# Kernel tuning notes

Hardware: AMD Instinct MI355X
Metric: run time of the kernel (lower is better)

## Reference

```python
import jax, jax.numpy as jnp
import numpy as np

N = 50000          # nodes
DEG = 8            # per-node in/out degree
E = N * DEG        # fwd edges (rev = reversed fwd)
H = 128            # hidden_dim
T = 4              # towers
F = H // T         # per-tower F_in (divide_input=True)
FO = H // T        # per-tower F_out
L = 2              # num_layers
IN_DIM = 128
OUT_DIM = 32
AVG_LOG = float(np.log(DEG + 1.0))  # avg of log(deg+1) from deg histogram (all deg==8)
BN_EPS = 1e-5
STD_EPS = 1e-5


def setup_inputs() -> dict:
    key = jax.random.key(0)
    ks = jax.random.split(key, 10)
    x = jax.random.normal(ks[0], (N, IN_DIM), jnp.float32)
    # every node appears exactly DEG times as dst and as src -> deg histogram delta at 8
    dst = jnp.repeat(jnp.arange(N, dtype=jnp.int32), DEG)
    src = jax.random.permutation(ks[1], dst)
    edge_fwd = jnp.stack([src, dst])  # [2, E]

    def rn(k, shape):
        return jax.random.normal(k, shape, jnp.float32) * 0.05

    return dict(
        x=x,
        W_in=rn(ks[2], (IN_DIM, H)), b_in=jnp.zeros((H,), jnp.float32),
        # [layer, relation(fwd/rev), tower, ...]
        pre_W=rn(ks[3], (L, 2, T, 2 * F, F)), pre_b=jnp.zeros((L, 2, T, F), jnp.float32),
        post_W=rn(ks[4], (L, 2, T, 13 * F, FO)), post_b=jnp.zeros((L, 2, T, FO), jnp.float32),
        lin_W=rn(ks[5], (L, 2, H, H)), lin_b=jnp.zeros((L, 2, H), jnp.float32),
        bn_gamma=jnp.ones((L, H), jnp.float32), bn_beta=jnp.zeros((L, H), jnp.float32),
        mlp_W1=rn(ks[6], (H, H)), mlp_b1=jnp.zeros((H,), jnp.float32),
        mlp_W2=rn(ks[7], (H, OUT_DIM)), mlp_b2=jnp.zeros((OUT_DIM,), jnp.float32),
        edge_fwd=edge_fwd,
    )


def _pna(x, src, dst, pre_W, pre_b, post_W, post_b, lin_W, lin_b):
    """One PNAConv (divide_input=True, pre/post_layers=1, no edge attr)."""
    xt = x.reshape(N, T, F)                                   # [N,T,F]
    # message: cat([x_i (dst), x_j (src)]) -> per-tower pre-MLP
    h = jnp.concatenate([xt[dst], xt[src]], axis=-1)          # [E,T,2F]
    m = jnp.einsum('etf,tfg->etg', h, pre_W) + pre_b          # [E,T,F]
    # multi-aggregator scatter reduce over destination nodes
    deg = jax.ops.segment_sum(jnp.ones((m.shape[0],), x.dtype), dst, N)
    degc = jnp.maximum(deg, 1.0)
    inv = (1.0 / degc)[:, None, None]
    mean = jax.ops.segment_sum(m, dst, N) * inv
    mean2 = jax.ops.segment_sum(m * m, dst, N) * inv
    std = jnp.sqrt(jax.nn.relu(mean2 - mean * mean) + STD_EPS)
    mn = jax.ops.segment_min(m, dst, N)
    mx = jax.ops.segment_max(m, dst, N)
    agg = jnp.concatenate([mean, mn, mx, std], axis=-1)       # [N,T,4F]
    # degree scalers: amplification, attenuation, identity
    ld = jnp.log(degc + 1.0)[:, None, None]
    agg = jnp.concatenate([agg * (ld / AVG_LOG), agg * (AVG_LOG / ld), agg], axis=-1)  # [N,T,12F]
    out = jnp.concatenate([xt, agg], axis=-1)                 # [N,T,13F]
    out = jnp.einsum('ntf,tfg->ntg', out, post_W) + post_b    # [N,T,FO]
    out = out.reshape(N, T * FO)
    return out @ lin_W + lin_b                                # [N,H]


def _bn(x, g, b):
    mu = x.mean(0)
    var = x.var(0)  # biased, as torch BatchNorm normalization
    return g * (x - mu) * jax.lax.rsqrt(var + BN_EPS) + b


def reference(x, W_in, b_in, pre_W, pre_b, post_W, post_b, lin_W, lin_b,
              bn_gamma, bn_beta, mlp_W1, mlp_b1, mlp_W2, mlp_b2, edge_fwd):
    src, dst = edge_fwd[0], edge_fwd[1]
    h = jax.nn.relu(x @ W_in + b_in)
    for l in range(L):
        # HeteroConv sum of fwd relation and rev relation (reversed edges)
        y = (_pna(h, src, dst, pre_W[l, 0], pre_b[l, 0], post_W[l, 0], post_b[l, 0], lin_W[l, 0], lin_b[l, 0])
             + _pna(h, dst, src, pre_W[l, 1], pre_b[l, 1], post_W[l, 1], post_b[l, 1], lin_W[l, 1], lin_b[l, 1]))
        h = jax.nn.relu(_bn(y, bn_gamma[l], bn_beta[l]))
        # dropout omitted (deterministic reference / eval mode)
    return jax.nn.relu(h @ mlp_W1 + mlp_b1) @ mlp_W2 + mlp_b2
```

## Files before the change

### kernel.cpp

```cpp
#include <hip/hip_runtime.h>
#include <hip/hip_fp16.h>
#include <cstddef>
#include <cstdint>

#define NN 50000
#define DEG 8
#define EE (NN*DEG)
#define RT_CNT 3125
#define KSTEPS 36
#define W8L 18432
#define MPAD 132

typedef __attribute__((ext_vector_type(8))) short short8;
typedef __attribute__((ext_vector_type(4))) float f32x4;

union Pack8 { __half h[8]; __half2 h2[4]; uint4 u; short8 s8; };

__global__ void k_build_nbr(const int* __restrict__ ef, int* __restrict__ cnt,
                            int* __restrict__ fwd_nbr, int* __restrict__ rev_nbr) {
    int e = blockIdx.x * blockDim.x + threadIdx.x;
    if (e >= EE) return;
    int s = ef[e], d = ef[EE + e];
    int p = atomicAdd(&cnt[d], 1);
    fwd_nbr[d * DEG + p] = s;
    int q = atomicAdd(&cnt[NN + s], 1);
    rev_nbr[s * DEG + q] = d;
}

__global__ __launch_bounds__(256) void k_wprep(
    const float* __restrict__ post_W, const float* __restrict__ pre_W,
    const float* __restrict__ pre_b, const float* __restrict__ post_b,
    const float* __restrict__ lin_W, const float* __restrict__ lin_b,
    __half* __restrict__ Wcp, float* __restrict__ Qw, float* __restrict__ bc) {
    __shared__ float Pf[160 * 33];
    __shared__ float Wl[32 * 128];
    __shared__ float Wt[32 * 32];
    __shared__ float Ps[32 * 32];
    __shared__ float Q[32 * 32];
    __shared__ float T3s[32];
    int tid = threadIdx.x;
    int m4 = blockIdx.x;
    int l = m4 >> 3, r = (m4 >> 2) & 1, tw = m4 & 3;
    const float* PW = post_W + (size_t)m4 * 416 * 32;
    for (int i = tid; i < 160 * 32; i += 256) {
        int row = i >> 5, g = i & 31;
        float v;
        if (row < 32) v = PW[row * 32 + g];
        else {
            int rr = row - 32;
            v = PW[(32 + rr) * 32 + g] + PW[(160 + rr) * 32 + g] + PW[(288 + rr) * 32 + g];
        }
        Pf[row * 33 + g] = v;
    }
    for (int i = tid; i < 1024; i += 256) Wt[i] = pre_W[(size_t)m4 * 2048 + i];
    for (int i = tid; i < 4096; i += 256)
        Wl[i] = lin_W[(size_t)(l * 2 + r) * 16384 + tw * 32 * 128 + i];
    __syncthreads();
    for (int i = tid; i < 1024; i += 256) {
        int g = i >> 5, j = i & 31;
        Ps[i] = Pf[(32 + g) * 33 + j] + Pf[(64 + g) * 33 + j] + Pf[(96 + g) * 33 + j];
    }
    __syncthreads();
    for (int i = tid; i < 1024; i += 256) {
        int f = i >> 5, j = i & 31;
        float acc = Pf[f * 33 + j];
#pragma unroll
        for (int g = 0; g < 32; g++) acc += Wt[f * 32 + g] * Ps[g * 32 + j];
        Q[i] = acc;
    }
    if (tid < 32) {
        int j = tid;
        float v = post_b[m4 * 32 + j];
#pragma unroll
        for (int g = 0; g < 32; g++) v += pre_b[m4 * 32 + g] * Ps[g * 32 + j];
        T3s[j] = v;
    }
    __syncthreads();
    for (int u = tid; u < 2048; u += 256) {
        int lane = u & 63, t = (u >> 6) & 7, s = u >> 9;
        int quad = lane >> 4, nl = lane & 15;
        int n = t * 16 + nl;
        Pack8 pk;
#pragma unroll
        for (int e = 0; e < 8; e++) {
            int f = quad * 8 + e;
            const float* Pr = &Pf[((s + 1) * 32 + f) * 33];
            float acc = 0.f;
#pragma unroll
            for (int j = 0; j < 32; j++) acc += Pr[j] * Wl[j * 128 + n];
            pk.h[e] = __float2half(acc);
        }
        int ks = 4 + r * 16 + tw * 4 + s;
        *(uint4*)&Wcp[((size_t)l * W8L + (t * KSTEPS + ks) * 64 + lane) * 8] = pk.u;
    }
    for (int i = tid; i < 4096; i += 256) {
        int f = i >> 7, n = i & 127;
        float acc = 0.f;
#pragma unroll
        for (int j = 0; j < 32; j++) acc += Q[f * 32 + j] * Wl[j * 128 + n];
        atomicAdd(&Qw[(size_t)l * 16384 + (tw * 32 + f) * 128 + n], acc);
    }
    if (tid < 128) {
        float v = 0.f;
#pragma unroll
        for (int j = 0; j < 32; j++) v += T3s[j] * Wl[j * 128 + tid];
        atomicAdd(&bc[l * 128 + tid], v);
        if ((m4 & 7) == 0)
            atomicAdd(&bc[l * 128 + tid],
                      lin_b[(2 * l) * 128 + tid] + lin_b[(2 * l + 1) * 128 + tid]);
    }
}

__global__ void k_pack_xt(const float* __restrict__ Qw, __half* __restrict__ Wcp) {
    int gid = blockIdx.x * blockDim.x + threadIdx.x;
    if (gid >= 2 * 4 * 8 * 64) return;
    int lane = gid & 63, t = (gid >> 6) & 7, ks = (gid >> 9) & 3, l = gid >> 11;
    int quad = lane >> 4;
    int n = t * 16 + (lane & 15);
    Pack8 pk;
#pragma unroll
    for (int e = 0; e < 8; e++)
        pk.h[e] = __float2half(Qw[(size_t)l * 16384 + (ks * 32 + quad * 8 + e) * 128 + n]);
    *(uint4*)&Wcp[((size_t)l * W8L + (t * KSTEPS + ks) * 64 + lane) * 8] = pk.u;
}

__global__ void k_pack_b(const float* __restrict__ W, int K, int N,
                         __half* __restrict__ dst) {
    int gid = blockIdx.x * blockDim.x + threadIdx.x;
    int total = (K >> 5) * (N >> 4) * 64;
    if (gid >= total) return;
    int lane = gid & 63;
    int ks = (gid >> 6) % (K >> 5);
    int t = (gid >> 6) / (K >> 5);
    int quad = lane >> 4, nl = lane & 15;
    int n = t * 16 + nl;
    Pack8 pk;
#pragma unroll
    for (int e = 0; e < 8; e++)
        pk.h[e] = __float2half(W[(size_t)(ks * 32 + quad * 8 + e) * N + n]);
    *(uint4*)&dst[(size_t)gid * 8] = pk.u;
}

__global__ void k_pack_wbd(const float* __restrict__ pre_W, __half* __restrict__ dst) {
    int gid = blockIdx.x * blockDim.x + threadIdx.x;
    if (gid >= 2 * 2 * 8 * 4 * 64) return;
    int lane = gid & 63, ks = (gid >> 6) & 3, t8 = (gid >> 8) & 7;
    int rel = (gid >> 11) & 1, l = gid >> 12;
    int quad = lane >> 4, nl = lane & 15;
    int n = t8 * 16 + nl;
    int tn = n >> 5;
    Pack8 pk;
#pragma unroll
    for (int e = 0; e < 8; e++) {
        int k = ks * 32 + quad * 8 + e;
        float v = 0.f;
        if ((k >> 5) == tn)
            v = pre_W[(size_t)((((l * 2 + rel) * 4 + tn) * 64) + 32 + (k & 31)) * 32 + (n & 31)];
        pk.h[e] = __float2half(v);
    }
    *(uint4*)&dst[((size_t)(l * 2 + rel) * 2048 + (t8 * 4 + ks) * 64 + lane) * 8] = pk.u;
}

__global__ __launch_bounds__(256) void k_in_mfma(
    const float* __restrict__ X, const __half* __restrict__ Wp,
    const float* __restrict__ b, __half* __restrict__ H) {
    __shared__ __half Sh[4][16 * MPAD];
    int tid = threadIdx.x, wv = tid >> 6, lane = tid & 63;
    int rt = blockIdx.x * 4 + wv;
    if (rt >= RT_CNT) rt = RT_CNT - 1;
    int mm = lane & 15, quad = lane >> 4;
    short8 a[4];
#pragma unroll
    for (int ks = 0; ks < 4; ks++) {
        const float4* p = (const float4*)&X[(size_t)(rt * 16 + mm) * 128 + ks * 32 + quad * 8];
        float4 v0 = p[0], v1 = p[1];
        Pack8 pk;
        pk.h[0] = __float2half(v0.x); pk.h[1] = __float2half(v0.y);
        pk.h[2] = __float2half(v0.z); pk.h[3] = __float2half(v0.w);
        pk.h[4] = __float2half(v1.x); pk.h[5] = __float2half(v1.y);
        pk.h[6] = __float2half(v1.z); pk.h[7] = __float2half(v1.w);
        a[ks] = pk.s8;
    }
    const short8* Bb = (const short8*)Wp + lane;
    f32x4 acc[8];
#pragma unroll
    for (int t = 0; t < 8; t++) acc[t] = (f32x4){0.f, 0.f, 0.f, 0.f};
#pragma unroll
    for (int ks = 0; ks < 4; ks++)
#pragma unroll
        for (int t = 0; t < 8; t++)
            acc[t] = __builtin_amdgcn_mfma_f32_16x16x32_f16(
                a[ks], Bb[(t * 4 + ks) * 64], acc[t], 0, 0, 0);
    __half* T = Sh[wv];
#pragma unroll
    for (int t = 0; t < 8; t++) {
        int n = t * 16 + mm;
        float bias = b[n];
#pragma unroll
        for (int r = 0; r < 4; r++)
            T[(quad * 4 + r) * MPAD + n] = __float2half(fmaxf(acc[t][r] + bias, 0.f));
    }
#pragma unroll
    for (int it = 0; it < 4; it++) {
        int idx = it * 64 + lane;
        int row = idx >> 4, col = (idx & 15) * 8;
        *(uint4*)&H[(size_t)(rt * 16 + row) * 128 + col] = *(uint4*)&T[row * MPAD + col];
    }
}

template<int V>
__global__ __launch_bounds__(256) void k_preB_mfma(
    const __half* __restrict__ Hin, const float* __restrict__ Yf,
    const float* __restrict__ bns, const float* __restrict__ bns2,
    const float* __restrict__ gamma, const float* __restrict__ beta,
    __half* __restrict__ Hout, const __half* __restrict__ WbBDp,
    __half* __restrict__ Bplanes) {
    __shared__ __half Sh[4][16 * MPAD];
    __shared__ float sc[128], sh[128];
    int tid = threadIdx.x, wv = tid >> 6, lane = tid & 63;
    int rt = blockIdx.x * 4 + wv;
    if (rt >= RT_CNT) rt = RT_CNT - 1;
    if (V == 2) {
        if (tid < 128) {
            float mu = bns[tid] * (1.f / NN);
            float var = bns2[tid] * (1.f / NN) - mu * mu;
            float s = gamma[tid] * rsqrtf(var + 1e-5f);
            sc[tid] = s;
            sh[tid] = beta[tid] - mu * s;
        }
        __syncthreads();
    }
    int mm = lane & 15, quad = lane >> 4;
    short8 a[4];
#pragma unroll
    for (int ks = 0; ks < 4; ks++) {
        int c0 = ks * 32 + quad * 8;
        size_t base = (size_t)(rt * 16 + mm) * 128 + c0;
        if (V == 1) {
            Pack8 pk; pk.u = *(const uint4*)&Hin[base];
            a[ks] = pk.s8;
        } else {
            const float4* p = (const float4*)&Yf[base];
            float4 v0 = p[0], v1 = p[1];
            float4 s0 = *(const float4*)&sc[c0], s1 = *(const float4*)&sc[c0 + 4];
            float4 f0 = *(const float4*)&sh[c0], f1 = *(const float4*)&sh[c0 + 4];
            Pack8 pk;
            pk.h[0] = __float2half(fmaxf(s0.x * v0.x + f0.x, 0.f));
            pk.h[1] = __float2half(fmaxf(s0.y * v0.y + f0.y, 0.f));
            pk.h[2] = __float2half(fmaxf(s0.z * v0.z + f0.z, 0.f));
            pk.h[3] = __float2half(fmaxf(s0.w * v0.w + f0.w, 0.f));
            pk.h[4] = __float2half(fmaxf(s1.x * v1.x + f1.x, 0.f));
            pk.h[5] = __float2half(fmaxf(s1.y * v1.y + f1.y, 0.f));
            pk.h[6] = __float2half(fmaxf(s1.z * v1.z + f1.z, 0.f));
            pk.h[7] = __float2half(fmaxf(s1.w * v1.w + f1.w, 0.f));
            *(uint4*)&Hout[base] = pk.u;
            a[ks] = pk.s8;
        }
    }
    __half* T = Sh[wv];
#pragma unroll
    for (int rel = 0; rel < 2; rel++) {
        const short8* Bb = (const short8*)WbBDp + (size_t)rel * 2048 + lane;
        f32x4 acc[8];
#pragma unroll
        for (int t = 0; t < 8; t++) acc[t] = (f32x4){0.f, 0.f, 0.f, 0.f};
#pragma unroll
        for (int ks = 0; ks < 4; ks++)
#pragma unroll
            for (int t = 0; t < 8; t++)
                acc[t] = __builtin_amdgcn_mfma_f32_16x16x32_f16(
                    a[ks], Bb[(t * 4 + ks) * 64], acc[t], 0, 0, 0);
#pragma unroll
        for (int t = 0; t < 8; t++) {
            int n = t * 16 + mm;
#pragma unroll
            for (int r = 0; r < 4; r++)
                T[(quad * 4 + r) * MPAD + n] = __float2half(acc[t][r]);
        }
        __half* Bp = Bplanes + (size_t)rel * NN * 128;
#pragma unroll
        for (int it = 0; it < 4; it++) {
            int idx = it * 64 + lane;
            int row = idx >> 4, col = (idx & 15) * 8;
            *(uint4*)&Bp[(size_t)(rt * 16 + row) * 128 + col] = *(uint4*)&T[row * MPAD + col];
        }
    }
}

__global__ __launch_bounds__(256, 4) void k_agg_gemm(
    const __half* __restrict__ hbuf, const __half* __restrict__ Bplanes,
    const int* __restrict__ fwd_nbr, const int* __restrict__ rev_nbr,
    const __half* __restrict__ Wcp, const float* __restrict__ bc,
    float* __restrict__ Y, float* __restrict__ bnsum, float* __restrict__ bnsum2) {
    __shared__ __half Spack[KSTEPS * 64 * 8];
    __shared__ float bnred[256];
    int tid = threadIdx.x;
    int blk = blockIdx.x;
    bnred[tid] = 0.f;
    int lane = tid & 63, wv = tid >> 6;
    int s = lane >> 4, f16 = lane & 15;
    int tw = f16 >> 2, quad = f16 & 3;
    int m = wv * 4 + s;
    int d = blk * 16 + m;
    {
        const int4* nf = (const int4*)&fwd_nbr[d * 8];
        const int4* nr = (const int4*)&rev_nbr[d * 8];
        int4 a0 = nf[0], a1 = nf[1], b0v = nr[0], b1v = nr[1];
        int idx0[8] = {a0.x, a0.y, a0.z, a0.w, a1.x, a1.y, a1.z, a1.w};
        int idx1[8] = {b0v.x, b0v.y, b0v.z, b0v.w, b1v.x, b1v.y, b1v.z, b1v.w};
        int fo = f16 * 8;
        Pack8 r0[8], r1[8];
        const __half* Bp1 = Bplanes + (size_t)NN * 128;
#pragma unroll
        for (int k = 0; k < 8; k++)
            r0[k].u = *(const uint4*)&Bplanes[(size_t)idx0[k] * 128 + fo];
#pragma unroll
        for (int k = 0; k < 8; k++)
            r1[k].u = *(const uint4*)&Bp1[(size_t)idx1[k] * 128 + fo];
        Pack8 xr;
        xr.u = *(const uint4*)&hbuf[(size_t)(blk * 16 + f16) * 128 + wv * 32 + s * 8];
        int pos = 16 * quad + (m ^ quad ^ ((tw & 1) << 2));
#pragma unroll
        for (int rel = 0; rel < 2; rel++) {
            Pack8* rr = rel ? r1 : r0;
            float sS[8], qS[8], mnS[8], mxS[8];
#pragma unroll
            for (int j = 0; j < 8; j++) {
                sS[j] = 0.f; qS[j] = 0.f; mnS[j] = 1e30f; mxS[j] = -1e30f;
            }
#pragma unroll
            for (int k = 0; k < 8; k++) {
#pragma unroll
                for (int j2 = 0; j2 < 4; j2++) {
                    __half2 h = rr[k].h2[j2];
                    float a = __half2float(__low2half(h));
                    float b = __half2float(__high2half(h));
                    int j0 = 2 * j2, j1 = j0 + 1;
                    sS[j0] += a; qS[j0] += a * a;
                    mnS[j0] = fminf(mnS[j0], a); mxS[j0] = fmaxf(mxS[j0], a);
                    sS[j1] += b; qS[j1] += b * b;
                    mnS[j1] = fminf(mnS[j1], b); mxS[j1] = fmaxf(mxS[j1], b);
                }
            }
            Pack8 mean, stdv, mnp, mxp;
#pragma unroll
            for (int j = 0; j < 8; j++) {
                float Bm = sS[j] * 0.125f;
                mean.h[j] = __float2half(Bm);
                stdv.h[j] = __float2half(
                    sqrtf(fmaxf(qS[j] * 0.125f - Bm * Bm, 0.f) + 1e-5f));
                mnp.h[j] = __float2half(mnS[j]);
                mxp.h[j] = __float2half(mxS[j]);
            }
            int ksb = 4 + rel * 16 + tw * 4;
            *(uint4*)&Spack[((size_t)(ksb + 0) * 64 + pos) * 8] = mean.u;
            *(uint4*)&Spack[((size_t)(ksb + 1) * 64 + pos) * 8] = mnp.u;
            *(uint4*)&Spack[((size_t)(ksb + 2) * 64 + pos) * 8] = mxp.u;
            *(uint4*)&Spack[((size_t)(ksb + 3) * 64 + pos) * 8] = stdv.u;
        }
        int posx = 16 * s + (f16 ^ s ^ ((wv & 1) << 2));
        *(uint4*)&Spack[((size_t)wv * 64 + posx) * 8] = xr.u;
    }
    __syncthreads();
    int mB = lane & 15, qB = lane >> 4;
    int t0 = wv * 2;
    const short8* Bb = (const short8*)Wcp + lane;
    f32x4 acc0 = (f32x4){0.f, 0.f, 0.f, 0.f};
    f32x4 acc1 = (f32x4){0.f, 0.f, 0.f, 0.f};
    short8 p0[6], p1[6];
#pragma unroll
    for (int dd = 0; dd < 6; dd++) {
        p0[dd] = Bb[((size_t)t0 * KSTEPS + dd) * 64];
        p1[dd] = Bb[((size_t)(t0 + 1) * KSTEPS + dd) * 64];
    }
#pragma unroll
    for (int ks = 0; ks < KSTEPS; ks++) {
        int twk = (ks < 4) ? ks : (((ks - 4) >> 2) & 3);
        int posr = 16 * qB + (mB ^ qB ^ ((twk & 1) << 2));
        short8 a = *(const short8*)&Spack[((size_t)ks * 64 + posr) * 8];
        acc0 = __builtin_amdgcn_mfma_f32_16x16x32_f16(a, p0[ks % 6], acc0, 0, 0, 0);
        acc1 = __builtin_amdgcn_mfma_f32_16x16x32_f16(a, p1[ks % 6], acc1, 0, 0, 0);
        if (ks + 6 < KSTEPS) {
            p0[ks % 6] = Bb[((size_t)t0 * KSTEPS + ks + 6) * 64];
            p1[ks % 6] = Bb[((size_t)(t0 + 1) * KSTEPS + ks + 6) * 64];
        }
    }
#pragma unroll
    for (int tt = 0; tt < 2; tt++) {
        f32x4 acc = tt ? acc1 : acc0;
        int n = (t0 + tt) * 16 + mB;
        float bias = bc[n];
        float ls = 0.f, ls2 = 0.f;
#pragma unroll
        for (int r = 0; r < 4; r++) {
            float v = acc[r] + bias;
            int node = blk * 16 + qB * 4 + r;
            Y[(size_t)node * 128 + n] = v;
            ls += v; ls2 += v * v;
        }
        ls += __shfl_xor(ls, 16); ls += __shfl_xor(ls, 32);
        ls2 += __shfl_xor(ls2, 16); ls2 += __shfl_xor(ls2, 32);
        if (qB == 0) { bnred[n] += ls; bnred[128 + n] += ls2; }
    }
    __syncthreads();
    if (tid < 128) {
        atomicAdd(&bnsum[tid], bnred[tid]);
        atomicAdd(&bnsum2[tid], bnred[128 + tid]);
    }
}

__global__ __launch_bounds__(256) void k_mlp_mfma(
    const float* __restrict__ Yb, const float* __restrict__ bns,
    const float* __restrict__ bns2, const float* __restrict__ gamma,
    const float* __restrict__ beta, const __half* __restrict__ W1p,
    const float* __restrict__ b1, const __half* __restrict__ W2p,
    const float* __restrict__ b2, float* __restrict__ out) {
    __shared__ __half Sh[4][16 * MPAD];
    __shared__ float sc[128], sh[128];
    int tid = threadIdx.x, wv = tid >> 6, lane = tid & 63;
    int rt = blockIdx.x * 4 + wv;
    if (rt >= RT_CNT) rt = RT_CNT - 1;
    if (tid < 128) {
        float mu = bns[tid] * (1.f / NN);
        float var = bns2[tid] * (1.f / NN) - mu * mu;
        float s = gamma[tid] * rsqrtf(var + 1e-5f);
        sc[tid] = s;
        sh[tid] = beta[tid] - mu * s;
    }
    __syncthreads();
    int mm = lane & 15, quad = lane >> 4;
    short8 a[4];
#pragma unroll
    for (int ks = 0; ks < 4; ks++) {
        int c0 = ks * 32 + quad * 8;
        const float4* p = (const float4*)&Yb[(size_t)(rt * 16 + mm) * 128 + c0];
        float4 v0 = p[0], v1 = p[1];
        float4 s0 = *(const float4*)&sc[c0], s1 = *(const float4*)&sc[c0 + 4];
        float4 f0 = *(const float4*)&sh[c0], f1 = *(const float4*)&sh[c0 + 4];
        Pack8 pk;
        pk.h[0] = __float2half(fmaxf(s0.x * v0.x + f0.x, 0.f));
        pk.h[1] = __float2half(fmaxf(s0.y * v0.y + f0.y, 0.f));
        pk.h[2] = __float2half(fmaxf(s0.z * v0.z + f0.z, 0.f));
        pk.h[3] = __float2half(fmaxf(s0.w * v0.w + f0.w, 0.f));
        pk.h[4] = __float2half(fmaxf(s1.x * v1.x + f1.x, 0.f));
        pk.h[5] = __float2half(fmaxf(s1.y * v1.y + f1.y, 0.f));
        pk.h[6] = __float2half(fmaxf(s1.z * v1.z + f1.z, 0.f));
        pk.h[7] = __float2half(fmaxf(s1.w * v1.w + f1.w, 0.f));
        a[ks] = pk.s8;
    }
    const short8* B1 = (const short8*)W1p + lane;
    f32x4 acc[8];
#pragma unroll
    for (int t = 0; t < 8; t++) acc[t] = (f32x4){0.f, 0.f, 0.f, 0.f};
#pragma unroll
    for (int ks = 0; ks < 4; ks++)
#pragma unroll
        for (int t = 0; t < 8; t++)
            acc[t] = __builtin_amdgcn_mfma_f32_16x16x32_f16(
                a[ks], B1[(t * 4 + ks) * 64], acc[t], 0, 0, 0);
    __half* T = Sh[wv];
#pragma unroll
    for (int t = 0; t < 8; t++) {
        int n = t * 16 + mm;
        float bias = b1[n];
#pragma unroll
        for (int r = 0; r < 4; r++)
            T[(quad * 4 + r) * MPAD + n] = __float2half(fmaxf(acc[t][r] + bias, 0.f));
    }
    short8 a2[4];
#pragma unroll
    for (int ks = 0; ks < 4; ks++)
        a2[ks] = *(const short8*)&T[mm * MPAD + ks * 32 + quad * 8];
    const short8* B2 = (const short8*)W2p + lane;
    f32x4 acc2[2];
#pragma unroll
    for (int t = 0; t < 2; t++) acc2[t] = (f32x4){0.f, 0.f, 0.f, 0.f};
#pragma unroll
    for (int ks = 0; ks < 4; ks++)
#pragma unroll
        for (int t = 0; t < 2; t++)
            acc2[t] = __builtin_amdgcn_mfma_f32_16x16x32_f16(
                a2[ks], B2[(t * 4 + ks) * 64], acc2[t], 0, 0, 0);
#pragma unroll
    for (int t = 0; t < 2; t++) {
        int n = t * 16 + mm;
        float bias = b2[n];
#pragma unroll
        for (int r = 0; r < 4; r++)
            out[(size_t)(rt * 16 + quad * 4 + r) * 32 + n] = acc2[t][r] + bias;
    }
}

extern "C" void kernel_launch(void* const* d_in, const int* in_sizes, int n_in,
                              void* d_out, int out_size, void* d_ws, size_t ws_size,
                              hipStream_t stream) {
    const float* x      = (const float*)d_in[0];
    const float* W_in   = (const float*)d_in[1];
    const float* b_in   = (const float*)d_in[2];
    const float* pre_W  = (const float*)d_in[3];
    const float* pre_b  = (const float*)d_in[4];
    const float* post_W = (const float*)d_in[5];
    const float* post_b = (const float*)d_in[6];
    const float* lin_W  = (const float*)d_in[7];
    const float* lin_b  = (const float*)d_in[8];
    const float* bn_g   = (const float*)d_in[9];
    const float* bn_b   = (const float*)d_in[10];
    const float* mlp_W1 = (const float*)d_in[11];
    const float* mlp_b1 = (const float*)d_in[12];
    const float* mlp_W2 = (const float*)d_in[13];
    const float* mlp_b2 = (const float*)d_in[14];
    const int*   edge   = (const int*)d_in[15];
    float* out = (float*)d_out;

    char* w = (char*)d_ws;
    const size_t plane = (size_t)NN * 128 * sizeof(float);
    __half* hbuf = (__half*)w; w += plane / 2;
    float* ybuf = (float*)w; w += plane;
    __half* Bpl = (__half*)w; w += plane;
    int* fwd_nbr = (int*)w; w += (size_t)NN * DEG * sizeof(int);
    int* rev_nbr = (int*)w; w += (size_t)NN * DEG * sizeof(int);
    int* cnt     = (int*)w; w += (size_t)2 * NN * sizeof(int);
    float* Qw    = (float*)w; w += (size_t)2 * 128 * 128 * sizeof(float);
    float* bc    = (float*)w; w += 2 * 128 * sizeof(float);
    __half* Wcp  = (__half*)w; w += (size_t)2 * KSTEPS * 32 * 128 * sizeof(__half);
    __half* Winp = (__half*)w; w += (size_t)128 * 128 * sizeof(__half);
    __half* W1p  = (__half*)w; w += (size_t)128 * 128 * sizeof(__half);
    __half* W2p  = (__half*)w; w += (size_t)128 * 32 * sizeof(__half);
    __half* WbBD = (__half*)w; w += (size_t)4 * 128 * 128 * sizeof(__half);
    float* bns   = (float*)w; w += 4 * 128 * sizeof(float);

    const int gWave = (RT_CNT + 3) / 4;

    (void)hipMemsetAsync(cnt, 0, (size_t)2 * NN * sizeof(int), stream);
    (void)hipMemsetAsync(Qw, 0, (size_t)(2 * 128 * 128 + 2 * 128) * sizeof(float), stream);
    (void)hipMemsetAsync(bns, 0, 4 * 128 * sizeof(float), stream);
    k_build_nbr<<<(EE + 255) / 256, 256, 0, stream>>>(edge, cnt, fwd_nbr, rev_nbr);
    k_wprep<<<16, 256, 0, stream>>>(post_W, pre_W, pre_b, post_b, lin_W, lin_b,
                                    Wcp, Qw, bc);
    k_pack_xt<<<16, 256, 0, stream>>>(Qw, Wcp);
    k_pack_b<<<8, 256, 0, stream>>>(W_in, 128, 128, Winp);
    k_pack_b<<<8, 256, 0, stream>>>(mlp_W1, 128, 128, W1p);
    k_pack_b<<<2, 256, 0, stream>>>(mlp_W2, 128, 32, W2p);
    k_pack_wbd<<<32, 256, 0, stream>>>(pre_W, WbBD);

    k_in_mfma<<<gWave, 256, 0, stream>>>(x, Winp, b_in, hbuf);

    k_preB_mfma<1><<<gWave, 256, 0, stream>>>(
        hbuf, nullptr, nullptr, nullptr, nullptr, nullptr, nullptr,
        WbBD, Bpl);
    k_agg_gemm<<<RT_CNT, 256, 0, stream>>>(
        hbuf, Bpl, fwd_nbr, rev_nbr, Wcp, bc, ybuf, bns, bns + 128);
    k_preB_mfma<2><<<gWave, 256, 0, stream>>>(
        nullptr, ybuf, bns, bns + 128, bn_g, bn_b, hbuf,
        WbBD + (size_t)2 * 128 * 128, Bpl);
    k_agg_gemm<<<RT_CNT, 256, 0, stream>>>(
        hbuf, Bpl, fwd_nbr, rev_nbr, Wcp + (size_t)KSTEPS * 32 * 128,
        bc + 128, ybuf, bns + 256, bns + 384);

    k_mlp_mfma<<<gWave, 256, 0, stream>>>(ybuf, bns + 256, bns + 384,
                                          bn_g + 128, bn_b + 128,
                                          W1p, mlp_b1, W2p, mlp_b2, out);
}
```

Measured before the change: 457.5 us.

## Make aggregation GEMM kernel persistent with prefetch of next tile's neighbor gathers

The aggregation+GEMM kernel becomes a persistent grid of 1024 blocks that loops over row tiles. The neighbor indices and gathered rows for the next tile are loaded while the current tile's statistics and MFMA work run, hiding gather latency. BN partial sums now accumulate across tiles in shared memory, so there are fewer global atomics. The weight prefetch depth drops from 6 to 4 to save registers, and s_setprio is raised around the MFMA loop. The trade-off is higher register pressure from holding the prefetched rows, and possible load imbalance because 3125 tiles do not divide evenly over 1024 blocks.

```diff
diff --git a/kernel.cpp b/kernel.cpp
--- a/kernel.cpp
+++ b/kernel.cpp
@@ -10,6 +10,7 @@
 #define KSTEPS 36
 #define W8L 18432
 #define MPAD 132
+#define GRID_B 1024
 
 typedef __attribute__((ext_vector_type(8))) short short8;
 typedef __attribute__((ext_vector_type(4))) float f32x4;
@@ -295,31 +296,48 @@
     __shared__ __half Spack[KSTEPS * 64 * 8];
     __shared__ float bnred[256];
     int tid = threadIdx.x;
-    int blk = blockIdx.x;
     bnred[tid] = 0.f;
     int lane = tid & 63, wv = tid >> 6;
     int s = lane >> 4, f16 = lane & 15;
     int tw = f16 >> 2, quad = f16 & 3;
     int m = wv * 4 + s;
-    int d = blk * 16 + m;
+    int fo = f16 * 8;
+    int pos = 16 * quad + (m ^ quad ^ ((tw & 1) << 2));
+    int posx = 16 * s + (f16 ^ s ^ ((wv & 1) << 2));
+    int mB = lane & 15, qB = lane >> 4;
+    int t0 = wv * 2;
+    const __half* Bp1 = Bplanes + (size_t)NN * 128;
+    const short8* Bb = (const short8*)Wcp + lane;
+    float bias0 = bc[t0 * 16 + mB];
+    float bias1 = bc[(t0 + 1) * 16 + mB];
+
+    Pack8 r0[8], r1[8], xr;
     {
+        int d = blockIdx.x * 16 + m;
         const int4* nf = (const int4*)&fwd_nbr[d * 8];
         const int4* nr = (const int4*)&rev_nbr[d * 8];
         int4 a0 = nf[0], a1 = nf[1], b0v = nr[0], b1v = nr[1];
-        int idx0[8] = {a0.x, a0.y, a0.z, a0.w, a1.x, a1.y, a1.z, a1.w};
-        int idx1[8] = {b0v.x, b0v.y, b0v.z, b0v.w, b1v.x, b1v.y, b1v.z, b1v.w};
-        int fo = f16 * 8;
-        Pack8 r0[8], r1[8];
-        const __half* Bp1 = Bplanes + (size_t)NN * 128;
+        int i0[8] = {a0.x, a0.y, a0.z, a0.w, a1.x, a1.y, a1.z, a1.w};
+        int i1[8] = {b0v.x, b0v.y, b0v.z, b0v.w, b1v.x, b1v.y, b1v.z, b1v.w};
 #pragma unroll
         for (int k = 0; k < 8; k++)
-            r0[k].u = *(const uint4*)&Bplanes[(size_t)idx0[k] * 128 + fo];
+            r0[k].u = *(const uint4*)&Bplanes[(size_t)i0[k] * 128 + fo];
 #pragma unroll
         for (int k = 0; k < 8; k++)
-            r1[k].u = *(const uint4*)&Bp1[(size_t)idx1[k] * 128 + fo];
-        Pack8 xr;
-        xr.u = *(const uint4*)&hbuf[(size_t)(blk * 16 + f16) * 128 + wv * 32 + s * 8];
-        int pos = 16 * quad + (m ^ quad ^ ((tw & 1) << 2));
+            r1[k].u = *(const uint4*)&Bp1[(size_t)i1[k] * 128 + fo];
+        xr.u = *(const uint4*)&hbuf[(size_t)(blockIdx.x * 16 + f16) * 128 + wv * 32 + s * 8];
+    }
+
+    for (int tile = blockIdx.x; tile < RT_CNT; tile += GRID_B) {
+        int nt = tile + GRID_B;
+        bool hn = nt < RT_CNT;
+        int4 na0, na1, nb0, nb1;
+        if (hn) {
+            int dn = nt * 16 + m;
+            const int4* nf = (const int4*)&fwd_nbr[dn * 8];
+            const int4* nr = (const int4*)&rev_nbr[dn * 8];
+            na0 = nf[0]; na1 = nf[1]; nb0 = nr[0]; nb1 = nr[1];
+        }
 #pragma unroll
         for (int rel = 0; rel < 2; rel++) {
             Pack8* rr = rel ? r1 : r0;
@@ -358,51 +376,59 @@
             *(uint4*)&Spack[((size_t)(ksb + 2) * 64 + pos) * 8] = mxp.u;
             *(uint4*)&Spack[((size_t)(ksb + 3) * 64 + pos) * 8] = stdv.u;
         }
-        int posx = 16 * s + (f16 ^ s ^ ((wv & 1) << 2));
         *(uint4*)&Spack[((size_t)wv * 64 + posx) * 8] = xr.u;
-    }
-    __syncthreads();
-    int mB = lane & 15, qB = lane >> 4;
-    int t0 = wv * 2;
-    const short8* Bb = (const short8*)Wcp + lane;
-    f32x4 acc0 = (f32x4){0.f, 0.f, 0.f, 0.f};
-    f32x4 acc1 = (f32x4){0.f, 0.f, 0.f, 0.f};
-    short8 p0[6], p1[6];
-#pragma unroll
-    for (int dd = 0; dd < 6; dd++) {
-        p0[dd] = Bb[((size_t)t0 * KSTEPS + dd) * 64];
-        p1[dd] = Bb[((size_t)(t0 + 1) * KSTEPS + dd) * 64];
-    }
-#pragma unroll
-    for (int ks = 0; ks < KSTEPS; ks++) {
-        int twk = (ks < 4) ? ks : (((ks - 4) >> 2) & 3);
-        int posr = 16 * qB + (mB ^ qB ^ ((twk & 1) << 2));
-        short8 a = *(const short8*)&Spack[((size_t)ks * 64 + posr) * 8];
-        acc0 = __builtin_amdgcn_mfma_f32_16x16x32_f16(a, p0[ks % 6], acc0, 0, 0, 0);
-        acc1 = __builtin_amdgcn_mfma_f32_16x16x32_f16(a, p1[ks % 6], acc1, 0, 0, 0);
-        if (ks + 6 < KSTEPS) {
-            p0[ks % 6] = Bb[((size_t)t0 * KSTEPS + ks + 6) * 64];
-            p1[ks % 6] = Bb[((size_t)(t0 + 1) * KSTEPS + ks + 6) * 64];
-        }
-    }
-#pragma unroll
-    for (int tt = 0; tt < 2; tt++) {
-        f32x4 acc = tt ? acc1 : acc0;
-        int n = (t0 + tt) * 16 + mB;
-        float bias = bc[n];
-        float ls = 0.f, ls2 = 0.f;
-#pragma unroll
-        for (int r = 0; r < 4; r++) {
-            float v = acc[r] + bias;
-            int node = blk * 16 + qB * 4 + r;
-            Y[(size_t)node * 128 + n] = v;
-            ls += v; ls2 += v * v;
-        }
-        ls += __shfl_xor(ls, 16); ls += __shfl_xor(ls, 32);
-        ls2 += __shfl_xor(ls2, 16); ls2 += __shfl_xor(ls2, 32);
-        if (qB == 0) { bnred[n] += ls; bnred[128 + n] += ls2; }
-    }
-    __syncthreads();
+        if (hn) {
+            int i0[8] = {na0.x, na0.y, na0.z, na0.w, na1.x, na1.y, na1.z, na1.w};
+            int i1[8] = {nb0.x, nb0.y, nb0.z, nb0.w, nb1.x, nb1.y, nb1.z, nb1.w};
+#pragma unroll
+            for (int k = 0; k < 8; k++)
+                r0[k].u = *(const uint4*)&Bplanes[(size_t)i0[k] * 128 + fo];
+#pragma unroll
+            for (int k = 0; k < 8; k++)
+                r1[k].u = *(const uint4*)&Bp1[(size_t)i1[k] * 128 + fo];
+            xr.u = *(const uint4*)&hbuf[(size_t)(nt * 16 + f16) * 128 + wv * 32 + s * 8];
+        }
+        __syncthreads();
+        f32x4 acc0 = (f32x4){0.f, 0.f, 0.f, 0.f};
+        f32x4 acc1 = (f32x4){0.f, 0.f, 0.f, 0.f};
+        short8 p0[4], p1[4];
+#pragma unroll
+        for (int dd = 0; dd < 4; dd++) {
+            p0[dd] = Bb[((size_t)t0 * KSTEPS + dd) * 64];
+            p1[dd] = Bb[((size_t)(t0 + 1) * KSTEPS + dd) * 64];
+        }
+        __builtin_amdgcn_s_setprio(1);
+#pragma unroll
+        for (int ks = 0; ks < KSTEPS; ks++) {
+            int twk = (ks < 4) ? ks : (((ks - 4) >> 2) & 3);
+            int posr = 16 * qB + (mB ^ qB ^ ((twk & 1) << 2));
+            short8 a = *(const short8*)&Spack[((size_t)ks * 64 + posr) * 8];
+            acc0 = __builtin_amdgcn_mfma_f32_16x16x32_f16(a, p0[ks & 3], acc0, 0, 0, 0);
+            acc1 = __builtin_amdgcn_mfma_f32_16x16x32_f16(a, p1[ks & 3], acc1, 0, 0, 0);
+            if (ks + 4 < KSTEPS) {
+                p0[ks & 3] = Bb[((size_t)t0 * KSTEPS + ks + 4) * 64];
+                p1[ks & 3] = Bb[((size_t)(t0 + 1) * KSTEPS + ks + 4) * 64];
+            }
+        }
+        __builtin_amdgcn_s_setprio(0);
+#pragma unroll
+        for (int tt = 0; tt < 2; tt++) {
+            f32x4 acc = tt ? acc1 : acc0;
+            int n = (t0 + tt) * 16 + mB;
+            float bias = tt ? bias1 : bias0;
+            float ls = 0.f, ls2 = 0.f;
+#pragma unroll
+            for (int r = 0; r < 4; r++) {
+                float v = acc[r] + bias;
+                Y[(size_t)(tile * 16 + qB * 4 + r) * 128 + n] = v;
+                ls += v; ls2 += v * v;
+            }
+            ls += __shfl_xor(ls, 16); ls += __shfl_xor(ls, 32);
+            ls2 += __shfl_xor(ls2, 16); ls2 += __shfl_xor(ls2, 32);
+            if (qB == 0) { bnred[n] += ls; bnred[128 + n] += ls2; }
+        }
+        __syncthreads();
+    }
     if (tid < 128) {
         atomicAdd(&bnsum[tid], bnred[tid]);
         atomicAdd(&bnsum2[tid], bnred[128 + tid]);
@@ -484,7 +510,7 @@
 #pragma unroll
     for (int t = 0; t < 2; t++) {
         int n = t * 16 + mm;
-        float bias = b2[n];
+        float bias = b2[t * 16 + mm];
 #pragma unroll
         for (int r = 0; r < 4; r++)
             out[(size_t)(rt * 16 + quad * 4 + r) * 32 + n] = acc2[t][r] + bias;
@@ -548,12 +574,12 @@
     k_preB_mfma<1><<<gWave, 256, 0, stream>>>(
         hbuf, nullptr, nullptr, nullptr, nullptr, nullptr, nullptr,
         WbBD, Bpl);
-    k_agg_gemm<<<RT_CNT, 256, 0, stream>>>(
+    k_agg_gemm<<<GRID_B, 256, 0, stream>>>(
         hbuf, Bpl, fwd_nbr, rev_nbr, Wcp, bc, ybuf, bns, bns + 128);
     k_preB_mfma<2><<<gWave, 256, 0, stream>>>(
         nullptr, ybuf, bns, bns + 128, bn_g, bn_b, hbuf,
         WbBD + (size_t)2 * 128 * 128, Bpl);
-    k_agg_gemm<<<RT_CNT, 256, 0, stream>>>(
+    k_agg_gemm<<<GRID_B, 256, 0, stream>>>(
         hbuf, Bpl, fwd_nbr, rev_nbr, Wcp + (size_t)KSTEPS * 32 * 128,
         bc + 128, ybuf, bns + 256, bns + 384);
 
```

Result: slower. 1.041 ms (+127.6%).

## Fuse input projection with first pre-MLP and trim agg kernel shared memory

Applied to the files above, without the earlier changes.

Fuses the input projection kernel with the first-layer pre-transform GEMM, so the freshly computed hidden tile is reused from shared memory and one launch plus one reread of hbuf are removed. In the aggregation GEMM, the node's own features are loaded straight into registers as MFMA A-operands rather than staged through shared memory, which shrinks the LDS buffer, and the occupancy hint is raised from 4 to 5 blocks. The block-level BN reduction array and its barrier are replaced by direct global atomics from each wave, and MFMA loop priority is raised with s_setprio. The trade-off is more global atomic traffic and higher register pressure from the extra A registers under a tighter launch bound.

```diff
diff --git a/kernel.cpp b/kernel.cpp
--- a/kernel.cpp
+++ b/kernel.cpp
@@ -161,9 +161,10 @@
     *(uint4*)&dst[((size_t)(l * 2 + rel) * 2048 + (t8 * 4 + ks) * 64 + lane) * 8] = pk.u;
 }
 
-__global__ __launch_bounds__(256) void k_in_mfma(
+__global__ __launch_bounds__(256) void k_in_fused(
     const float* __restrict__ X, const __half* __restrict__ Wp,
-    const float* __restrict__ b, __half* __restrict__ H) {
+    const float* __restrict__ b, const __half* __restrict__ WbBDp,
+    __half* __restrict__ H, __half* __restrict__ Bplanes) {
     __shared__ __half Sh[4][16 * MPAD];
     int tid = threadIdx.x, wv = tid >> 6, lane = tid & 63;
     int rt = blockIdx.x * 4 + wv;
@@ -205,6 +206,37 @@
         int idx = it * 64 + lane;
         int row = idx >> 4, col = (idx & 15) * 8;
         *(uint4*)&H[(size_t)(rt * 16 + row) * 128 + col] = *(uint4*)&T[row * MPAD + col];
+    }
+    short8 a2[4];
+#pragma unroll
+    for (int ks = 0; ks < 4; ks++)
+        a2[ks] = *(const short8*)&T[mm * MPAD + ks * 32 + quad * 8];
+#pragma unroll
+    for (int rel = 0; rel < 2; rel++) {
+        const short8* Bd = (const short8*)WbBDp + (size_t)rel * 2048 + lane;
+        f32x4 ac[8];
+#pragma unroll
+        for (int t = 0; t < 8; t++) ac[t] = (f32x4){0.f, 0.f, 0.f, 0.f};
+#pragma unroll
+        for (int ks = 0; ks < 4; ks++)
+#pragma unroll
+            for (int t = 0; t < 8; t++)
+                ac[t] = __builtin_amdgcn_mfma_f32_16x16x32_f16(
+                    a2[ks], Bd[(t * 4 + ks) * 64], ac[t], 0, 0, 0);
+#pragma unroll
+        for (int t = 0; t < 8; t++) {
+            int n = t * 16 + mm;
+#pragma unroll
+            for (int r = 0; r < 4; r++)
+                T[(quad * 4 + r) * MPAD + n] = __float2half(ac[t][r]);
+        }
+        __half* Bp = Bplanes + (size_t)rel * NN * 128;
+#pragma unroll
+        for (int it = 0; it < 4; it++) {
+            int idx = it * 64 + lane;
+            int row = idx >> 4, col = (idx & 15) * 8;
+            *(uint4*)&Bp[(size_t)(rt * 16 + row) * 128 + col] = *(uint4*)&T[row * MPAD + col];
+        }
     }
 }
 
@@ -287,21 +319,24 @@
     }
 }
 
-__global__ __launch_bounds__(256, 4) void k_agg_gemm(
+__global__ __launch_bounds__(256, 5) void k_agg_gemm(
     const __half* __restrict__ hbuf, const __half* __restrict__ Bplanes,
     const int* __restrict__ fwd_nbr, const int* __restrict__ rev_nbr,
     const __half* __restrict__ Wcp, const float* __restrict__ bc,
     float* __restrict__ Y, float* __restrict__ bnsum, float* __restrict__ bnsum2) {
-    __shared__ __half Spack[KSTEPS * 64 * 8];
-    __shared__ float bnred[256];
+    __shared__ __half Spack[32 * 64 * 8];
     int tid = threadIdx.x;
     int blk = blockIdx.x;
-    bnred[tid] = 0.f;
     int lane = tid & 63, wv = tid >> 6;
     int s = lane >> 4, f16 = lane & 15;
     int tw = f16 >> 2, quad = f16 & 3;
     int m = wv * 4 + s;
     int d = blk * 16 + m;
+    int mB = lane & 15, qB = lane >> 4;
+    Pack8 axt[4];
+#pragma unroll
+    for (int ks = 0; ks < 4; ks++)
+        axt[ks].u = *(const uint4*)&hbuf[(size_t)(blk * 16 + mB) * 128 + ks * 32 + qB * 8];
     {
         const int4* nf = (const int4*)&fwd_nbr[d * 8];
         const int4* nr = (const int4*)&rev_nbr[d * 8];
@@ -317,8 +352,6 @@
 #pragma unroll
         for (int k = 0; k < 8; k++)
             r1[k].u = *(const uint4*)&Bp1[(size_t)idx1[k] * 128 + fo];
-        Pack8 xr;
-        xr.u = *(const uint4*)&hbuf[(size_t)(blk * 16 + f16) * 128 + wv * 32 + s * 8];
         int pos = 16 * quad + (m ^ quad ^ ((tw & 1) << 2));
 #pragma unroll
         for (int rel = 0; rel < 2; rel++) {
@@ -352,17 +385,14 @@
                 mnp.h[j] = __float2half(mnS[j]);
                 mxp.h[j] = __float2half(mxS[j]);
             }
-            int ksb = 4 + rel * 16 + tw * 4;
+            int ksb = rel * 16 + tw * 4;
             *(uint4*)&Spack[((size_t)(ksb + 0) * 64 + pos) * 8] = mean.u;
             *(uint4*)&Spack[((size_t)(ksb + 1) * 64 + pos) * 8] = mnp.u;
             *(uint4*)&Spack[((size_t)(ksb + 2) * 64 + pos) * 8] = mxp.u;
             *(uint4*)&Spack[((size_t)(ksb + 3) * 64 + pos) * 8] = stdv.u;
         }
-        int posx = 16 * s + (f16 ^ s ^ ((wv & 1) << 2));
-        *(uint4*)&Spack[((size_t)wv * 64 + posx) * 8] = xr.u;
     }
     __syncthreads();
-    int mB = lane & 15, qB = lane >> 4;
     int t0 = wv * 2;
     const short8* Bb = (const short8*)Wcp + lane;
     f32x4 acc0 = (f32x4){0.f, 0.f, 0.f, 0.f};
@@ -373,11 +403,18 @@
         p0[dd] = Bb[((size_t)t0 * KSTEPS + dd) * 64];
         p1[dd] = Bb[((size_t)(t0 + 1) * KSTEPS + dd) * 64];
     }
+    __builtin_amdgcn_s_setprio(1);
 #pragma unroll
     for (int ks = 0; ks < KSTEPS; ks++) {
-        int twk = (ks < 4) ? ks : (((ks - 4) >> 2) & 3);
-        int posr = 16 * qB + (mB ^ qB ^ ((twk & 1) << 2));
-        short8 a = *(const short8*)&Spack[((size_t)ks * 64 + posr) * 8];
+        short8 a;
+        if (ks < 4) {
+            a = axt[ks].s8;
+        } else {
+            int ss = ks - 4;
+            int twk = (ss >> 2) & 3;
+            int posr = 16 * qB + (mB ^ qB ^ ((twk & 1) << 2));
+            a = *(const short8*)&Spack[((size_t)ss * 64 + posr) * 8];
+        }
         acc0 = __builtin_amdgcn_mfma_f32_16x16x32_f16(a, p0[ks % 6], acc0, 0, 0, 0);
         acc1 = __builtin_amdgcn_mfma_f32_16x16x32_f16(a, p1[ks % 6], acc1, 0, 0, 0);
         if (ks + 6 < KSTEPS) {
@@ -385,6 +422,7 @@
             p1[ks % 6] = Bb[((size_t)(t0 + 1) * KSTEPS + ks + 6) * 64];
         }
     }
+    __builtin_amdgcn_s_setprio(0);
 #pragma unroll
     for (int tt = 0; tt < 2; tt++) {
         f32x4 acc = tt ? acc1 : acc0;
@@ -400,12 +438,10 @@
         }
         ls += __shfl_xor(ls, 16); ls += __shfl_xor(ls, 32);
         ls2 += __shfl_xor(ls2, 16); ls2 += __shfl_xor(ls2, 32);
-        if (qB == 0) { bnred[n] += ls; bnred[128 + n] += ls2; }
-    }
-    __syncthreads();
-    if (tid < 128) {
-        atomicAdd(&bnsum[tid], bnred[tid]);
-        atomicAdd(&bnsum2[tid], bnred[128 + tid]);
+        if (qB == 0) {
+            atomicAdd(&bnsum[n], ls);
+            atomicAdd(&bnsum2[n], ls2);
+        }
     }
 }
 
@@ -543,11 +579,8 @@
     k_pack_b<<<2, 256, 0, stream>>>(mlp_W2, 128, 32, W2p);
     k_pack_wbd<<<32, 256, 0, stream>>>(pre_W, WbBD);
 
-    k_in_mfma<<<gWave, 256, 0, stream>>>(x, Winp, b_in, hbuf);
-
-    k_preB_mfma<1><<<gWave, 256, 0, stream>>>(
-        hbuf, nullptr, nullptr, nullptr, nullptr, nullptr, nullptr,
-        WbBD, Bpl);
+    k_in_fused<<<gWave, 256, 0, stream>>>(x, Winp, b_in, WbBD, hbuf, Bpl);
+
     k_agg_gemm<<<RT_CNT, 256, 0, stream>>>(
         hbuf, Bpl, fwd_nbr, rev_nbr, Wcp, bc, ybuf, bns, bns + 128);
     k_preB_mfma<2><<<gWave, 256, 0, stream>>>(
```

New measurement: 454.9 us. Within noise of the previous version (-0.6%).
